# Kernel optimization log

Hardware: AMD Instinct MI355X
Metric: run time of the kernel (lower is better)

## Reference

```python
import jax, jax.numpy as jnp
import numpy as np

R_CUT = 5.0
N_NODES = 50000
N_EDGES = 400000
N_GRAPHS = 2500
D = 128        # embedding_size (hardcoded by torch.split(..., 128))
N_RBF = 20
N_BLOCKS = 3
PI = 3.141592653589793


def setup_inputs() -> dict:
    key = jax.random.key(0)
    ks = jax.random.split(key, 32)
    w = lambda k, s: (jax.random.normal(k, s) * 0.05).astype(jnp.float32)
    z = jax.random.randint(ks[0], (N_NODES,), 0, 100)
    edges = jax.random.randint(ks[1], (N_EDGES, 2), 0, N_NODES)
    r_ij = jax.random.uniform(ks[2], (N_EDGES, 1), minval=0.8, maxval=R_CUT, dtype=jnp.float32)
    d = jax.random.normal(ks[3], (N_EDGES, 3), dtype=jnp.float32)
    r_ij_normalized = d / jnp.linalg.norm(d, axis=1, keepdims=True)
    graph_idx = jax.random.randint(ks[4], (N_NODES,), 0, N_GRAPHS)
    return {
        "z": z, "edges": edges, "r_ij": r_ij,
        "r_ij_normalized": r_ij_normalized, "graph_idx": graph_idx,
        "emb": w(ks[5], (100, D)),
        # message blocks (stacked over N_BLOCKS)
        "msg_w1": w(ks[6], (N_BLOCKS, D, D)),   "msg_b1": w(ks[7], (N_BLOCKS, D)),
        "msg_w2": w(ks[8], (N_BLOCKS, D, 3 * D)), "msg_b2": w(ks[9], (N_BLOCKS, 3 * D)),
        "rbf_w": w(ks[10], (N_BLOCKS, N_RBF, 3 * D)), "rbf_b": w(ks[11], (N_BLOCKS, 3 * D)),
        # update blocks
        "upd_U": w(ks[12], (N_BLOCKS, D, D)), "upd_V": w(ks[13], (N_BLOCKS, D, D)),
        "upd_w1": w(ks[14], (N_BLOCKS, 2 * D, D)), "upd_b1": w(ks[15], (N_BLOCKS, D)),
        "upd_w2": w(ks[16], (N_BLOCKS, D, 3 * D)), "upd_b2": w(ks[17], (N_BLOCKS, 3 * D)),
        # readout
        "blue_w1": w(ks[18], (D, D)), "blue_b1": w(ks[19], (D,)),
        "blue_w2": w(ks[20], (D, 1)), "blue_b2": w(ks[21], (1,)),
    }


def _rbf(r, r_cut):
    n = jnp.arange(1, N_RBF + 1, dtype=r.dtype)  # [20]
    return jnp.sin(n * PI / r_cut * r) / r        # [E,20]


def _fcut(r, r_cut):
    return jnp.where(r <= r_cut, 0.5 * (jnp.cos(PI * r / r_cut) + 1.0), 0.0)


def painn_forward(z, edges, r_ij, r_ij_normalized, graph_idx, emb,
                  msg_w1, msg_b1, msg_w2, msg_b2, rbf_w, rbf_b,
                  upd_U, upd_V, upd_w1, upd_b1, upd_w2, upd_b2,
                  blue_w1, blue_b1, blue_w2, blue_b2):
    silu = jax.nn.silu
    src = edges[:, 1]  # gathered (neighbor j)
    dst = edges[:, 0]  # scattered (center i)
    s = emb[z]                                           # [N,128]
    v = jnp.zeros((s.shape[0], 3, D), dtype=r_ij.dtype)  # [N,3,128]
    rbf = _rbf(r_ij, R_CUT)                              # [E,20]
    f_c = _fcut(r_ij, R_CUT)                             # [E,1]
    for i in range(N_BLOCKS):
        # --- message block ---
        rbf_fcut = (rbf @ rbf_w[i] + rbf_b[i]) * f_c            # [E,384]
        s_pass = silu(s @ msg_w1[i] + msg_b1[i]) @ msg_w2[i] + msg_b2[i]  # [N,384]
        pass_out = rbf_fcut * s_pass[src]                        # [E,384]
        d_v, d_s, d_rep = jnp.split(pass_out, 3, axis=-1)        # each [E,128]
        delta_v = v[src] * d_v[:, None, :] + r_ij_normalized[:, :, None] * d_rep[:, None, :]
        s = s + jax.ops.segment_sum(d_s, dst, num_segments=N_NODES)
        v = v + jax.ops.segment_sum(delta_v, dst, num_segments=N_NODES)
        # --- update block ---
        U_v = jnp.einsum('nde,ef->ndf', v, upd_U[i])             # [N,3,128]
        V_v = jnp.einsum('nde,ef->ndf', v, upd_V[i])
        V_norm = jnp.linalg.norm(V_v, axis=1)                    # [N,128]
        sv = jnp.concatenate([V_norm, s], axis=1)                # [N,256]
        a = silu(sv @ upd_w1[i] + upd_b1[i]) @ upd_w2[i] + upd_b2[i]  # [N,384]
        avv, asv, ass = jnp.split(a, 3, axis=1)
        s = s + jnp.sum(U_v * V_v, axis=1) * asv + ass
        v = v + avv[:, None, :] * U_v
    blue = silu(s @ blue_w1 + blue_b1) @ blue_w2 + blue_b2       # [N,1]
    return jax.ops.segment_sum(blue, graph_idx, num_segments=N_GRAPHS)  # [G,1]


def reference(z, edges, r_ij, r_ij_normalized, graph_idx, emb,
              msg_w1, msg_b1, msg_w2, msg_b2, rbf_w, rbf_b,
              upd_U, upd_V, upd_w1, upd_b1, upd_w2, upd_b2,
              blue_w1, blue_b1, blue_w2, blue_b2):
    return painn_forward(z, edges, r_ij, r_ij_normalized, graph_idx, emb,
                         msg_w1, msg_b1, msg_w2, msg_b2, rbf_w, rbf_b,
                         upd_U, upd_V, upd_w1, upd_b1, upd_w2, upd_b2,
                         blue_w1, blue_b1, blue_w2, blue_b2)
```

## Files before the change

### kernel.cpp

```cpp
#include <hip/hip_runtime.h>
#include <hip/hip_bf16.h>
#include <math.h>

#define N_NODES 50000
#define N_EDGES 400000
#define N_GRAPHS 2500
#define D 128
#define D3 384
#define N_RBF 20
#define R_CUT 5.0f
#define PI_F 3.14159265358979f
#define NCH 98
#define GEB 16
#define GLDS_STRIDE 388

typedef __attribute__((ext_vector_type(8))) short bf16x8;
typedef __attribute__((ext_vector_type(4))) float f32x4;

__device__ __forceinline__ float silu_f(float x) {
    return x / (1.0f + __expf(-x));
}
__device__ __forceinline__ short f2bf(float x) {
    union { float f; unsigned u; } v; v.f = x;
    unsigned r = (v.u + 0x7FFFu + ((v.u >> 16) & 1u)) >> 16;
    return (short)r;
}
__device__ __forceinline__ float bf2f(short x) {
    union { unsigned u; float f; } v; v.u = ((unsigned)(unsigned short)x) << 16;
    return v.f;
}

#define MAXJOBS 19
struct PackJobs {
    const float* W[MAXJOBS];
    short* P[MAXJOBS];
    int K[MAXJOBS];
    int N[MAXJOBS];
    int boff[MAXJOBS + 1];
    int njobs;
};
__global__ void k_packall(PackJobs jobs) {
    int b = blockIdx.x;
    int j = 0;
    while (j + 1 < jobs.njobs && b >= jobs.boff[j + 1]) ++j;
    int t = (b - jobs.boff[j]) * 256 + threadIdx.x;
    int K = jobs.K[j], N = jobs.N[j];
    int NKT = K / 32;
    int total = (N / 16) * NKT * 64;
    if (t >= total) return;
    const float* W = jobs.W[j];
    short* P = jobs.P[j];
    int lane = t & 63;
    int kt = (t >> 6) % NKT;
    int nt = (t >> 6) / NKT;
    int k0 = kt * 32 + (lane >> 4) * 8;
    int col = nt * 16 + (lane & 15);
    #pragma unroll
    for (int q = 0; q < 8; ++q)
        P[(size_t)t * 8 + q] = f2bf(W[(size_t)(k0 + q) * N + col]);
}

__global__ void k_packrbf(const float* __restrict__ rbf_w, const float* __restrict__ rbf_b,
                          short* __restrict__ P) {
    int t = blockIdx.x * 256 + threadIdx.x;
    if (t >= 3 * 1536) return;
    int i = t / 1536;
    int r = t - i * 1536;
    int lane = r & 63;
    int nt = r >> 6;
    int col = nt * 16 + (lane & 15);
    int k0 = (lane >> 4) * 8;
    const float* W = rbf_w + (size_t)i * N_RBF * D3;
    const float* B = rbf_b + (size_t)i * D3;
    short* out = P + (size_t)i * 12288 + (size_t)r * 8;
    #pragma unroll
    for (int q = 0; q < 8; ++q) {
        int k = k0 + q;
        float v = (k < N_RBF) ? W[(size_t)k * D3 + col] : ((k == N_RBF) ? B[col] : 0.0f);
        out[q] = f2bf(v);
    }
}

template<int K, int N, bool SILU, int AMODE>
__global__ __launch_bounds__(256) void k_gemm(const void* __restrict__ Aptr,
                                              const void* __restrict__ A2ptr,
                                              const short* __restrict__ Bp,
                                              const float* __restrict__ bias,
                                              short* __restrict__ Cbf, int M) {
    constexpr int NKT = K / 32, NNT = N / 16;
    int lane = threadIdx.x & 63, wv = threadIdx.x >> 6;
    int tile = blockIdx.x * 4 + wv;
    if (tile * 16 >= M) return;
    int arow = tile * 16 + (lane & 15);
    int kgrp = (lane >> 4) * 8;

    bf16x8 a[NKT];
    if (AMODE == 0) {
        const short* A = (const short*)Aptr + (size_t)arow * K + kgrp;
        #pragma unroll
        for (int kt = 0; kt < NKT; ++kt) a[kt] = *(const bf16x8*)(A + kt * 32);
    } else if (AMODE == 1) {
        const float* A = (const float*)Aptr + (size_t)arow * K + kgrp;
        #pragma unroll
        for (int kt = 0; kt < NKT; ++kt)
            #pragma unroll
            for (int j = 0; j < 8; ++j) a[kt][j] = f2bf(A[kt * 32 + j]);
    } else {
        const short* A1 = (const short*)Aptr + (size_t)arow * 128 + kgrp;
        const float* A2 = (const float*)A2ptr + (size_t)arow * 128 + kgrp;
        #pragma unroll
        for (int kt = 0; kt < 4 && kt < NKT; ++kt) a[kt] = *(const bf16x8*)(A1 + kt * 32);
        #pragma unroll
        for (int kt = 4; kt < NKT; ++kt)
            #pragma unroll
            for (int j = 0; j < 8; ++j) a[kt][j] = f2bf(A2[(kt - 4) * 32 + j]);
    }

    int crow0 = tile * 16 + (lane >> 4) * 4;
    int ccol = lane & 15;
    const bf16x8* Bv = (const bf16x8*)Bp;
    #pragma unroll
    for (int nt = 0; nt < NNT; ++nt) {
        f32x4 acc = {0.f, 0.f, 0.f, 0.f};
        #pragma unroll
        for (int kt = 0; kt < NKT; ++kt) {
            bf16x8 b = Bv[(nt * NKT + kt) * 64 + lane];
            acc = __builtin_amdgcn_mfma_f32_16x16x32_bf16(a[kt], b, acc, 0, 0, 0);
        }
        int col = nt * 16 + ccol;
        float bs = bias ? bias[col] : 0.0f;
        #pragma unroll
        for (int j = 0; j < 4; ++j) {
            float v = acc[j] + bs;
            if (SILU) v = silu_f(v);
            Cbf[(size_t)(crow0 + j) * N + col] = f2bf(v);
        }
    }
}

__global__ __launch_bounds__(256) void k_gemmUV(const short* __restrict__ A,
                                                const short* __restrict__ Bp,
                                                short* __restrict__ Cu,
                                                short* __restrict__ Cv, int M) {
    int lane = threadIdx.x & 63, wv = threadIdx.x >> 6;
    int tile = blockIdx.x * 4 + wv;
    if (tile * 16 >= M) return;
    int arow = tile * 16 + (lane & 15);
    int kgrp = (lane >> 4) * 8;
    const short* Ar = A + (size_t)arow * 128 + kgrp;
    bf16x8 a[4];
    #pragma unroll
    for (int kt = 0; kt < 4; ++kt) a[kt] = *(const bf16x8*)(Ar + kt * 32);
    int crow0 = tile * 16 + (lane >> 4) * 4;
    int ccol = lane & 15;
    const bf16x8* Bv = (const bf16x8*)Bp;
    #pragma unroll
    for (int nt = 0; nt < 16; ++nt) {
        f32x4 acc = {0.f, 0.f, 0.f, 0.f};
        #pragma unroll
        for (int kt = 0; kt < 4; ++kt)
            acc = __builtin_amdgcn_mfma_f32_16x16x32_bf16(a[kt], Bv[(nt * 4 + kt) * 64 + lane], acc, 0, 0, 0);
        int col = nt * 16 + ccol;
        short* C = (col < 128) ? Cu : Cv;
        int cc = col & 127;
        #pragma unroll
        for (int j = 0; j < 4; ++j)
            C[(size_t)(crow0 + j) * 128 + cc] = f2bf(acc[j]);
    }
}

__global__ void k_embed(const int* __restrict__ z, const float* __restrict__ emb,
                        float* __restrict__ s) {
    int i = blockIdx.x * blockDim.x + threadIdx.x;
    if (i < N_NODES * D) {
        int n = i >> 7, c = i & 127;
        s[i] = emb[z[n] * D + c];
    }
}

__global__ void k_hist(const int* __restrict__ edges, int* __restrict__ cnt) {
    int e = blockIdx.x * 256 + threadIdx.x;
    if (e < N_EDGES) atomicAdd(&cnt[edges[2 * e]], 1);
}

__global__ void k_scan1(const int* __restrict__ cnt, int* __restrict__ csum) {
    int t = threadIdx.x;
    int g = blockIdx.x * 512 + t;
    int v = (g < N_NODES) ? cnt[g] : 0;
    #pragma unroll
    for (int off = 32; off > 0; off >>= 1) v += __shfl_down(v, off, 64);
    __shared__ int ws[8];
    if ((t & 63) == 0) ws[t >> 6] = v;
    __syncthreads();
    if (t == 0) {
        int sum = 0;
        #pragma unroll
        for (int i = 0; i < 8; ++i) sum += ws[i];
        csum[blockIdx.x] = sum;
    }
}

__global__ void k_scan2(const int* __restrict__ csum, int* __restrict__ cbase) {
    if (threadIdx.x == 0 && blockIdx.x == 0) {
        int s = 0;
        for (int i = 0; i < NCH; ++i) { cbase[i] = s; s += csum[i]; }
    }
}

__global__ void k_scan3(const int* __restrict__ cnt, const int* __restrict__ cbase,
                        int* __restrict__ rowptr) {
    __shared__ int buf[512];
    int t = threadIdx.x;
    int g = blockIdx.x * 512 + t;
    int orig = (g < N_NODES) ? cnt[g] : 0;
    buf[t] = orig;
    __syncthreads();
    for (int off = 1; off < 512; off <<= 1) {
        int v = (t >= off) ? buf[t - off] : 0;
        __syncthreads();
        buf[t] += v;
        __syncthreads();
    }
    if (g < N_NODES) rowptr[g] = cbase[blockIdx.x] + buf[t] - orig;
    if (g == 0 && blockIdx.x == 0) rowptr[N_NODES] = N_EDGES;
}

__global__ void k_scatter(const int* __restrict__ edges, const float* __restrict__ r_ij,
                          const float* __restrict__ rhat, const int* __restrict__ rowptr,
                          int* __restrict__ cursor, int* __restrict__ esrc,
                          short* __restrict__ erbf, float4* __restrict__ erhat) {
    int e = blockIdx.x * 256 + threadIdx.x;
    if (e >= N_EDGES) return;
    int dst = edges[2 * e], src = edges[2 * e + 1];
    int p = rowptr[dst] + atomicAdd(&cursor[dst], 1);
    esrc[p] = src;
    float r = r_ij[e];
    float fc = (r <= R_CUT) ? 0.5f * (cosf(PI_F * r / R_CUT) + 1.0f) : 0.0f;
    float inv_r = 1.0f / r;
    short rec[32];
    #pragma unroll
    for (int k = 0; k < N_RBF; ++k)
        rec[k] = f2bf(sinf((float)(k + 1) * (PI_F / R_CUT) * r) * inv_r * fc);
    rec[20] = f2bf(fc);
    #pragma unroll
    for (int k = 21; k < 32; ++k) rec[k] = 0;
    short* out = erbf + (size_t)p * 32;
    #pragma unroll
    for (int k = 0; k < 32; ++k) out[k] = rec[k];
    float4 rh;
    rh.x = rhat[3 * e]; rh.y = rhat[3 * e + 1]; rh.z = rhat[3 * e + 2]; rh.w = 0.f;
    erhat[p] = rh;
}

__global__ __launch_bounds__(128, 4) void k_edge3(
    const int* __restrict__ rowptr, const int* __restrict__ esrc,
    const short* __restrict__ erbf, const float4* __restrict__ erhat,
    const short* __restrict__ pRbf,
    const short* __restrict__ spass, const short* __restrict__ vold,
    float* __restrict__ s, short* __restrict__ vnew) {
    __shared__ short gate_lds[GEB * GLDS_STRIDE];
    __shared__ int   src_lds[GEB];
    __shared__ float4 rh_lds[GEB];
    int tid = threadIdx.x;
    int lane = tid & 63;
    int wv = tid >> 6;
    int c = tid;
    int ntb = wv * 12;
    bf16x8 bfr[12];
    #pragma unroll
    for (int t = 0; t < 12; ++t)
        bfr[t] = *(const bf16x8*)(pRbf + ((size_t)((ntb + t) * 64 + lane)) * 8);
    int r0 = (lane >> 4) * 4;
    int fcol = lane & 15;
    for (int n = blockIdx.x; n < N_NODES; n += gridDim.x) {
        int p0 = rowptr[n], p1 = rowptr[n + 1];
        float sa = 0.f, va0 = 0.f, va1 = 0.f, va2 = 0.f;
        for (int pb = p0; pb < p1; pb += GEB) {
            int erow = pb + (lane & 15);
            if (erow >= p1) erow = p1 - 1;
            bf16x8 afrag = *(const bf16x8*)(erbf + (size_t)erow * 32 + (lane >> 4) * 8);
            if (tid < GEB) {
                int p = pb + tid;
                if (p < p1) { src_lds[tid] = esrc[p]; rh_lds[tid] = erhat[p]; }
            }
            #pragma unroll
            for (int t = 0; t < 12; ++t) {
                f32x4 acc = {0.f, 0.f, 0.f, 0.f};
                acc = __builtin_amdgcn_mfma_f32_16x16x32_bf16(afrag, bfr[t], acc, 0, 0, 0);
                int col = (ntb + t) * 16 + fcol;
                #pragma unroll
                for (int j = 0; j < 4; ++j)
                    gate_lds[(r0 + j) * GLDS_STRIDE + col] = f2bf(acc[j]);
            }
            __syncthreads();
            int pe = (pb + GEB < p1) ? pb + GEB : p1;
            for (int p = pb; p < pe; ++p) {
                int src = src_lds[p - pb];
                float4 rh = rh_lds[p - pb];
                const short* g = gate_lds + (p - pb) * GLDS_STRIDE;
                float a0 = bf2f(g[c]);
                float a1 = bf2f(g[128 + c]);
                float a2 = bf2f(g[256 + c]);
                const short* sp = spass + (size_t)src * D3;
                float dv = a0 * bf2f(sp[c]);
                float ds = a1 * bf2f(sp[128 + c]);
                float dr = a2 * bf2f(sp[256 + c]);
                sa += ds;
                const short* vs = vold + (size_t)src * D3;
                va0 += bf2f(vs[c]) * dv + rh.x * dr;
                va1 += bf2f(vs[128 + c]) * dv + rh.y * dr;
                va2 += bf2f(vs[256 + c]) * dv + rh.z * dr;
            }
            __syncthreads();
        }
        s[(size_t)n * D + c] += sa;
        size_t vb = (size_t)n * D3;
        vnew[vb + c]       = f2bf(bf2f(vold[vb + c]) + va0);
        vnew[vb + 128 + c] = f2bf(bf2f(vold[vb + 128 + c]) + va1);
        vnew[vb + 256 + c] = f2bf(bf2f(vold[vb + 256 + c]) + va2);
    }
}

__global__ void k_svbuild(const short* __restrict__ Vv, short* __restrict__ Vn) {
    int i = blockIdx.x * 256 + threadIdx.x;
    int n = i >> 7, c = i & 127;
    float acc = 0.f;
    #pragma unroll
    for (int d = 0; d < 3; ++d) {
        float v = bf2f(Vv[(size_t)(n * 3 + d) * D + c]);
        acc += v * v;
    }
    Vn[i] = f2bf(sqrtf(acc));
}

__global__ void k_apply(float* __restrict__ s, short* __restrict__ v,
                        const short* __restrict__ Uv, const short* __restrict__ Vv,
                        const short* __restrict__ a_bf) {
    int i = blockIdx.x * 256 + threadIdx.x;
    int n = i >> 7, c = i & 127;
    float avv = bf2f(a_bf[(size_t)n * D3 + c]);
    float asv = bf2f(a_bf[(size_t)n * D3 + 128 + c]);
    float ass = bf2f(a_bf[(size_t)n * D3 + 256 + c]);
    float scal = 0.f;
    float uvr[3];
    #pragma unroll
    for (int d = 0; d < 3; ++d) {
        float u = bf2f(Uv[(size_t)(n * 3 + d) * D + c]);
        float vv = bf2f(Vv[(size_t)(n * 3 + d) * D + c]);
        uvr[d] = u;
        scal += u * vv;
    }
    s[i] += scal * asv + ass;
    #pragma unroll
    for (int d = 0; d < 3; ++d) {
        size_t idx = (size_t)n * D3 + d * 128 + c;
        v[idx] = f2bf(bf2f(v[idx]) + avv * uvr[d]);
    }
}

__global__ void k_blue_dot(const short* __restrict__ h, const int* __restrict__ graph_idx,
                           const float* __restrict__ w2, const float* __restrict__ b2,
                           float* __restrict__ out) {
    __shared__ float red[4];
    int c = threadIdx.x & 127;
    int n = blockIdx.x * 2 + (threadIdx.x >> 7);
    float val = bf2f(h[(size_t)n * D + c]) * w2[c];
    #pragma unroll
    for (int off = 32; off > 0; off >>= 1) val += __shfl_down(val, off, 64);
    if ((threadIdx.x & 63) == 0) red[threadIdx.x >> 6] = val;
    __syncthreads();
    if (threadIdx.x == 0)   atomicAdd(&out[graph_idx[n]], red[0] + red[1] + b2[0]);
    if (threadIdx.x == 128) atomicAdd(&out[graph_idx[n]], red[2] + red[3] + b2[0]);
}

static inline int gemm_grid(int M) { return (M / 16 + 3) / 4; }

extern "C" void kernel_launch(void* const* d_in, const int* in_sizes, int n_in,
                              void* d_out, int out_size, void* d_ws, size_t ws_size,
                              hipStream_t stream) {
    const int*   z         = (const int*)d_in[0];
    const int*   edges     = (const int*)d_in[1];
    const float* r_ij      = (const float*)d_in[2];
    const float* rhat      = (const float*)d_in[3];
    const int*   graph_idx = (const int*)d_in[4];
    const float* emb       = (const float*)d_in[5];
    const float* msg_w1    = (const float*)d_in[6];
    const float* msg_b1    = (const float*)d_in[7];
    const float* msg_w2    = (const float*)d_in[8];
    const float* msg_b2    = (const float*)d_in[9];
    const float* rbf_w     = (const float*)d_in[10];
    const float* rbf_b     = (const float*)d_in[11];
    const float* upd_U     = (const float*)d_in[12];
    const float* upd_V     = (const float*)d_in[13];
    const float* upd_w1    = (const float*)d_in[14];
    const float* upd_b1    = (const float*)d_in[15];
    const float* upd_w2    = (const float*)d_in[16];
    const float* upd_b2    = (const float*)d_in[17];
    const float* blue_w1   = (const float*)d_in[18];
    const float* blue_b1   = (const float*)d_in[19];
    const float* blue_w2   = (const float*)d_in[20];
    const float* blue_b2   = (const float*)d_in[21];
    float* out = (float*)d_out;

    char* ws = (char*)d_ws;
    size_t off = 0;
    auto alloc = [&](size_t bytes) { void* p = ws + off; off += (bytes + 255) & ~(size_t)255; return p; };

    float* s      = (float*)alloc((size_t)N_NODES * D * 4);
    short* bufV0  = (short*)alloc((size_t)N_NODES * D3 * 2);
    short* bufV1  = (short*)alloc((size_t)N_NODES * D3 * 2);
    short* shrd   = (short*)alloc((size_t)N_NODES * D3 * 2);
    short* hbuf   = (short*)alloc((size_t)N_NODES * D * 2);
    short* Vv     = (short*)alloc((size_t)N_NODES * D3 * 2);
    short* Vn     = shrd;
    int*    esrc   = (int*)alloc((size_t)N_EDGES * 4);
    short*  erbf   = (short*)alloc((size_t)N_EDGES * 32 * 2);
    float4* erhat  = (float4*)alloc((size_t)N_EDGES * 16);
    int*    rowptr = (int*)alloc((size_t)(N_NODES + 1) * 4);
    int*    cnt    = (int*)alloc((size_t)N_NODES * 4);
    int*    csum   = (int*)alloc(NCH * 4);
    int*    cbase  = (int*)alloc(NCH * 4);

    short* pBlue = (short*)alloc(16384 * 2);
    short* pRbfAll = (short*)alloc((size_t)3 * 12288 * 2);
    short* pMsgW1[3]; short* pMsgW2[3]; short* pUV[3]; short* pUpdW1[3]; short* pUpdW2[3];
    for (int i = 0; i < 3; ++i) {
        pMsgW1[i] = (short*)alloc(16384 * 2);
        pMsgW2[i] = (short*)alloc(49152 * 2);
        pUV[i]    = (short*)alloc(32768 * 2);
        pUpdW1[i] = (short*)alloc(32768 * 2);
        pUpdW2[i] = (short*)alloc(49152 * 2);
    }

    PackJobs jobs;
    jobs.njobs = 0;
    int bacc = 0;
    auto addjob = [&](const float* W, short* P, int K, int N) {
        int j = jobs.njobs++;
        jobs.W[j] = W; jobs.P[j] = P; jobs.K[j] = K; jobs.N[j] = N;
        jobs.boff[j] = bacc;
        int total = (N / 16) * (K / 32) * 64;
        bacc += (total + 255) / 256;
        jobs.boff[j + 1] = bacc;
    };
    addjob(blue_w1, pBlue, 128, 128);
    for (int i = 0; i < 3; ++i) {
        addjob(msg_w1 + (size_t)i * D * D,     pMsgW1[i], 128, 128);
        addjob(msg_w2 + (size_t)i * D * D3,    pMsgW2[i], 128, 384);
        addjob(upd_U  + (size_t)i * D * D,     pUV[i],          128, 128);
        addjob(upd_V  + (size_t)i * D * D,     pUV[i] + 16384,  128, 128);
        addjob(upd_w1 + (size_t)i * 2 * D * D, pUpdW1[i], 256, 128);
        addjob(upd_w2 + (size_t)i * D * D3,    pUpdW2[i], 128, 384);
    }
    k_packall<<<bacc, 256, 0, stream>>>(jobs);
    k_packrbf<<<18, 256, 0, stream>>>(rbf_w, rbf_b, pRbfAll);

    hipMemsetAsync(cnt, 0, (size_t)N_NODES * 4, stream);
    k_hist<<<(N_EDGES + 255) / 256, 256, 0, stream>>>(edges, cnt);
    k_scan1<<<NCH, 512, 0, stream>>>(cnt, csum);
    k_scan2<<<1, 64, 0, stream>>>(csum, cbase);
    k_scan3<<<NCH, 512, 0, stream>>>(cnt, cbase, rowptr);
    hipMemsetAsync(cnt, 0, (size_t)N_NODES * 4, stream);
    k_scatter<<<(N_EDGES + 255) / 256, 256, 0, stream>>>(edges, r_ij, rhat, rowptr, cnt,
                                                         esrc, erbf, erhat);

    hipMemsetAsync(bufV0, 0, (size_t)N_NODES * D3 * 2, stream);
    hipMemsetAsync(d_out, 0, (size_t)out_size * sizeof(float), stream);
    k_embed<<<(N_NODES * D) / 256, 256, 0, stream>>>(z, emb, s);

    const int gN  = gemm_grid(N_NODES);
    const int gN3 = gemm_grid(N_NODES * 3);

    for (int i = 0; i < 3; ++i) {
        short* vstate = (i & 1) ? bufV1 : bufV0;
        short* vscr   = (i & 1) ? bufV0 : bufV1;
        k_gemm<128, 128, true, 1><<<gN, 256, 0, stream>>>(
            s, nullptr, pMsgW1[i], msg_b1 + (size_t)i * D, hbuf, N_NODES);
        k_gemm<128, 384, false, 0><<<gN, 256, 0, stream>>>(
            hbuf, nullptr, pMsgW2[i], msg_b2 + (size_t)i * D3, shrd, N_NODES);
        k_edge3<<<4096, 128, 0, stream>>>(rowptr, esrc, erbf, erhat,
                                          pRbfAll + (size_t)i * 12288,
                                          shrd, vstate, s, vscr);
        k_gemmUV<<<gN3, 256, 0, stream>>>(vscr, pUV[i], vstate, Vv, N_NODES * 3);
        k_svbuild<<<(N_NODES * D) / 256, 256, 0, stream>>>(Vv, Vn);
        k_gemm<256, 128, true, 2><<<gN, 256, 0, stream>>>(
            Vn, s, pUpdW1[i], upd_b1 + (size_t)i * D, hbuf, N_NODES);
        k_gemm<128, 384, false, 0><<<gN, 256, 0, stream>>>(
            hbuf, nullptr, pUpdW2[i], upd_b2 + (size_t)i * D3, shrd, N_NODES);
        k_apply<<<(N_NODES * D) / 256, 256, 0, stream>>>(s, vscr, vstate, Vv, shrd);
    }

    k_gemm<128, 128, true, 1><<<gN, 256, 0, stream>>>(
        s, nullptr, pBlue, blue_b1, hbuf, N_NODES);
    k_blue_dot<<<N_NODES / 2, 256, 0, stream>>>(hbuf, graph_idx, blue_w2, blue_b2, out);
}
```

Baseline: 1.021 ms.

## Fuse vector norm into update GEMM and apply into second update GEMM

Computes the per-channel vector norm inside the first update GEMM's A-load, which removes the separate norm kernel. The second update GEMM is fused with the state-apply step, so the 384-wide intermediate is never written to memory. The message GEMM output and the edge gate LDS are interleaved so each edge loads two gate values with a single 32-bit access. Edge unit vectors are packed into the unused slots of the RBF record, which drops the separate rhat array. The edge grid is enlarged and the LDS stride changed, and the fused apply kernel does scattered per-element global reads and writes.

```diff
diff --git a/kernel.cpp b/kernel.cpp
--- a/kernel.cpp
+++ b/kernel.cpp
@@ -12,7 +12,7 @@
 #define PI_F 3.14159265358979f
 #define NCH 98
 #define GEB 16
-#define GLDS_STRIDE 388
+#define GS 392
 
 typedef __attribute__((ext_vector_type(8))) short bf16x8;
 typedef __attribute__((ext_vector_type(4))) float f32x4;
@@ -81,7 +81,7 @@
     }
 }
 
-template<int K, int N, bool SILU, int AMODE>
+template<int K, int N, bool SILU, int AMODE, int CMODE>
 __global__ __launch_bounds__(256) void k_gemm(const void* __restrict__ Aptr,
                                               const void* __restrict__ A2ptr,
                                               const short* __restrict__ Bp,
@@ -106,10 +106,19 @@
             #pragma unroll
             for (int j = 0; j < 8; ++j) a[kt][j] = f2bf(A[kt * 32 + j]);
     } else {
-        const short* A1 = (const short*)Aptr + (size_t)arow * 128 + kgrp;
+        const short* A1 = (const short*)Aptr + (size_t)arow * D3 + kgrp;
         const float* A2 = (const float*)A2ptr + (size_t)arow * 128 + kgrp;
         #pragma unroll
-        for (int kt = 0; kt < 4 && kt < NKT; ++kt) a[kt] = *(const bf16x8*)(A1 + kt * 32);
+        for (int kt = 0; kt < 4 && kt < NKT; ++kt) {
+            bf16x8 v0 = *(const bf16x8*)(A1 + kt * 32);
+            bf16x8 v1 = *(const bf16x8*)(A1 + kt * 32 + 128);
+            bf16x8 v2 = *(const bf16x8*)(A1 + kt * 32 + 256);
+            #pragma unroll
+            for (int j = 0; j < 8; ++j) {
+                float f0 = bf2f(v0[j]), f1 = bf2f(v1[j]), f2 = bf2f(v2[j]);
+                a[kt][j] = f2bf(sqrtf(f0 * f0 + f1 * f1 + f2 * f2));
+            }
+        }
         #pragma unroll
         for (int kt = 4; kt < NKT; ++kt)
             #pragma unroll
@@ -129,11 +138,12 @@
         }
         int col = nt * 16 + ccol;
         float bs = bias ? bias[col] : 0.0f;
+        int oidx = (CMODE == 1) ? (col < 256 ? (((col & 127) << 1) | (col >> 7)) : col) : col;
         #pragma unroll
         for (int j = 0; j < 4; ++j) {
             float v = acc[j] + bs;
             if (SILU) v = silu_f(v);
-            Cbf[(size_t)(crow0 + j) * N + col] = f2bf(v);
+            Cbf[(size_t)(crow0 + j) * N + oidx] = f2bf(v);
         }
     }
 }
@@ -166,6 +176,60 @@
         #pragma unroll
         for (int j = 0; j < 4; ++j)
             C[(size_t)(crow0 + j) * 128 + cc] = f2bf(acc[j]);
+    }
+}
+
+__global__ __launch_bounds__(256) void k_w2apply(const short* __restrict__ A,
+                                                 const short* __restrict__ Bp,
+                                                 const float* __restrict__ b2,
+                                                 const short* __restrict__ Uv,
+                                                 const short* __restrict__ Vv,
+                                                 float* __restrict__ s,
+                                                 short* __restrict__ v, int M) {
+    int lane = threadIdx.x & 63, wv = threadIdx.x >> 6;
+    int tile = blockIdx.x * 4 + wv;
+    if (tile * 16 >= M) return;
+    int arow = tile * 16 + (lane & 15);
+    int kgrp = (lane >> 4) * 8;
+    const short* Ar = A + (size_t)arow * 128 + kgrp;
+    bf16x8 a[4];
+    #pragma unroll
+    for (int kt = 0; kt < 4; ++kt) a[kt] = *(const bf16x8*)(Ar + kt * 32);
+    int crow0 = tile * 16 + (lane >> 4) * 4;
+    int ccol = lane & 15;
+    const bf16x8* Bv = (const bf16x8*)Bp;
+    #pragma unroll
+    for (int t = 0; t < 8; ++t) {
+        f32x4 accA = {0.f, 0.f, 0.f, 0.f};
+        f32x4 accS = {0.f, 0.f, 0.f, 0.f};
+        f32x4 accB = {0.f, 0.f, 0.f, 0.f};
+        #pragma unroll
+        for (int kt = 0; kt < 4; ++kt) {
+            accA = __builtin_amdgcn_mfma_f32_16x16x32_bf16(a[kt], Bv[(t * 4 + kt) * 64 + lane], accA, 0, 0, 0);
+            accS = __builtin_amdgcn_mfma_f32_16x16x32_bf16(a[kt], Bv[((t + 8) * 4 + kt) * 64 + lane], accS, 0, 0, 0);
+            accB = __builtin_amdgcn_mfma_f32_16x16x32_bf16(a[kt], Bv[((t + 16) * 4 + kt) * 64 + lane], accB, 0, 0, 0);
+        }
+        int c = t * 16 + ccol;
+        float bA = b2[c], bS = b2[128 + c], bB = b2[256 + c];
+        #pragma unroll
+        for (int j = 0; j < 4; ++j) {
+            int n = crow0 + j;
+            float avv = accA[j] + bA;
+            float asv = accS[j] + bS;
+            float ass = accB[j] + bB;
+            const short* Un = Uv + (size_t)n * D3;
+            const short* Vn = Vv + (size_t)n * D3;
+            short* vn = v + (size_t)n * D3;
+            float scal = 0.f;
+            #pragma unroll
+            for (int d = 0; d < 3; ++d) {
+                float u = bf2f(Un[d * 128 + c]);
+                float vv = bf2f(Vn[d * 128 + c]);
+                scal += u * vv;
+                vn[d * 128 + c] = f2bf(bf2f(vn[d * 128 + c]) + avv * u);
+            }
+            s[(size_t)n * D + c] += scal * asv + ass;
+        }
     }
 }
 
@@ -228,7 +292,7 @@
 __global__ void k_scatter(const int* __restrict__ edges, const float* __restrict__ r_ij,
                           const float* __restrict__ rhat, const int* __restrict__ rowptr,
                           int* __restrict__ cursor, int* __restrict__ esrc,
-                          short* __restrict__ erbf, float4* __restrict__ erhat) {
+                          short* __restrict__ erbf) {
     int e = blockIdx.x * 256 + threadIdx.x;
     if (e >= N_EDGES) return;
     int dst = edges[2 * e], src = edges[2 * e + 1];
@@ -242,23 +306,22 @@
     for (int k = 0; k < N_RBF; ++k)
         rec[k] = f2bf(sinf((float)(k + 1) * (PI_F / R_CUT) * r) * inv_r * fc);
     rec[20] = f2bf(fc);
-    #pragma unroll
-    for (int k = 21; k < 32; ++k) rec[k] = 0;
+    rec[21] = f2bf(rhat[3 * e]);
+    rec[22] = f2bf(rhat[3 * e + 1]);
+    rec[23] = f2bf(rhat[3 * e + 2]);
+    #pragma unroll
+    for (int k = 24; k < 32; ++k) rec[k] = 0;
     short* out = erbf + (size_t)p * 32;
     #pragma unroll
     for (int k = 0; k < 32; ++k) out[k] = rec[k];
-    float4 rh;
-    rh.x = rhat[3 * e]; rh.y = rhat[3 * e + 1]; rh.z = rhat[3 * e + 2]; rh.w = 0.f;
-    erhat[p] = rh;
 }
 
 __global__ __launch_bounds__(128, 4) void k_edge3(
     const int* __restrict__ rowptr, const int* __restrict__ esrc,
-    const short* __restrict__ erbf, const float4* __restrict__ erhat,
-    const short* __restrict__ pRbf,
+    const short* __restrict__ erbf, const short* __restrict__ pRbf,
     const short* __restrict__ spass, const short* __restrict__ vold,
     float* __restrict__ s, short* __restrict__ vnew) {
-    __shared__ short gate_lds[GEB * GLDS_STRIDE];
+    __shared__ short gate_lds[GEB * GS];
     __shared__ int   src_lds[GEB];
     __shared__ float4 rh_lds[GEB];
     int tid = threadIdx.x;
@@ -281,29 +344,36 @@
             bf16x8 afrag = *(const bf16x8*)(erbf + (size_t)erow * 32 + (lane >> 4) * 8);
             if (tid < GEB) {
                 int p = pb + tid;
-                if (p < p1) { src_lds[tid] = esrc[p]; rh_lds[tid] = erhat[p]; }
+                if (p < p1) {
+                    src_lds[tid] = esrc[p];
+                    const short* eb = erbf + (size_t)p * 32;
+                    rh_lds[tid] = make_float4(bf2f(eb[21]), bf2f(eb[22]), bf2f(eb[23]), 0.f);
+                }
             }
             #pragma unroll
             for (int t = 0; t < 12; ++t) {
                 f32x4 acc = {0.f, 0.f, 0.f, 0.f};
                 acc = __builtin_amdgcn_mfma_f32_16x16x32_bf16(afrag, bfr[t], acc, 0, 0, 0);
                 int col = (ntb + t) * 16 + fcol;
+                int oidx = (col < 256) ? (((col & 127) << 1) | (col >> 7)) : col;
                 #pragma unroll
                 for (int j = 0; j < 4; ++j)
-                    gate_lds[(r0 + j) * GLDS_STRIDE + col] = f2bf(acc[j]);
+                    gate_lds[(r0 + j) * GS + oidx] = f2bf(acc[j]);
             }
             __syncthreads();
             int pe = (pb + GEB < p1) ? pb + GEB : p1;
             for (int p = pb; p < pe; ++p) {
                 int src = src_lds[p - pb];
                 float4 rh = rh_lds[p - pb];
-                const short* g = gate_lds + (p - pb) * GLDS_STRIDE;
-                float a0 = bf2f(g[c]);
-                float a1 = bf2f(g[128 + c]);
+                const short* g = gate_lds + (p - pb) * GS;
+                unsigned gp = *(const unsigned*)(g + 2 * c);
+                float a0 = bf2f((short)(gp & 0xFFFF));
+                float a1 = bf2f((short)(gp >> 16));
                 float a2 = bf2f(g[256 + c]);
                 const short* sp = spass + (size_t)src * D3;
-                float dv = a0 * bf2f(sp[c]);
-                float ds = a1 * bf2f(sp[128 + c]);
+                unsigned spp = *(const unsigned*)(sp + 2 * c);
+                float dv = a0 * bf2f((short)(spp & 0xFFFF));
+                float ds = a1 * bf2f((short)(spp >> 16));
                 float dr = a2 * bf2f(sp[256 + c]);
                 sa += ds;
                 const short* vs = vold + (size_t)src * D3;
@@ -318,43 +388,6 @@
         vnew[vb + c]       = f2bf(bf2f(vold[vb + c]) + va0);
         vnew[vb + 128 + c] = f2bf(bf2f(vold[vb + 128 + c]) + va1);
         vnew[vb + 256 + c] = f2bf(bf2f(vold[vb + 256 + c]) + va2);
-    }
-}
-
-__global__ void k_svbuild(const short* __restrict__ Vv, short* __restrict__ Vn) {
-    int i = blockIdx.x * 256 + threadIdx.x;
-    int n = i >> 7, c = i & 127;
-    float acc = 0.f;
-    #pragma unroll
-    for (int d = 0; d < 3; ++d) {
-        float v = bf2f(Vv[(size_t)(n * 3 + d) * D + c]);
-        acc += v * v;
-    }
-    Vn[i] = f2bf(sqrtf(acc));
-}
-
-__global__ void k_apply(float* __restrict__ s, short* __restrict__ v,
-                        const short* __restrict__ Uv, const short* __restrict__ Vv,
-                        const short* __restrict__ a_bf) {
-    int i = blockIdx.x * 256 + threadIdx.x;
-    int n = i >> 7, c = i & 127;
-    float avv = bf2f(a_bf[(size_t)n * D3 + c]);
-    float asv = bf2f(a_bf[(size_t)n * D3 + 128 + c]);
-    float ass = bf2f(a_bf[(size_t)n * D3 + 256 + c]);
-    float scal = 0.f;
-    float uvr[3];
-    #pragma unroll
-    for (int d = 0; d < 3; ++d) {
-        float u = bf2f(Uv[(size_t)(n * 3 + d) * D + c]);
-        float vv = bf2f(Vv[(size_t)(n * 3 + d) * D + c]);
-        uvr[d] = u;
-        scal += u * vv;
-    }
-    s[i] += scal * asv + ass;
-    #pragma unroll
-    for (int d = 0; d < 3; ++d) {
-        size_t idx = (size_t)n * D3 + d * 128 + c;
-        v[idx] = f2bf(bf2f(v[idx]) + avv * uvr[d]);
     }
 }
 
@@ -409,13 +442,11 @@
     float* s      = (float*)alloc((size_t)N_NODES * D * 4);
     short* bufV0  = (short*)alloc((size_t)N_NODES * D3 * 2);
     short* bufV1  = (short*)alloc((size_t)N_NODES * D3 * 2);
-    short* shrd   = (short*)alloc((size_t)N_NODES * D3 * 2);
+    short* spassI = (short*)alloc((size_t)N_NODES * D3 * 2);
     short* hbuf   = (short*)alloc((size_t)N_NODES * D * 2);
     short* Vv     = (short*)alloc((size_t)N_NODES * D3 * 2);
-    short* Vn     = shrd;
     int*    esrc   = (int*)alloc((size_t)N_EDGES * 4);
     short*  erbf   = (short*)alloc((size_t)N_EDGES * 32 * 2);
-    float4* erhat  = (float4*)alloc((size_t)N_EDGES * 16);
     int*    rowptr = (int*)alloc((size_t)(N_NODES + 1) * 4);
     int*    cnt    = (int*)alloc((size_t)N_NODES * 4);
     int*    csum   = (int*)alloc(NCH * 4);
@@ -462,7 +493,7 @@
     k_scan3<<<NCH, 512, 0, stream>>>(cnt, cbase, rowptr);
     hipMemsetAsync(cnt, 0, (size_t)N_NODES * 4, stream);
     k_scatter<<<(N_EDGES + 255) / 256, 256, 0, stream>>>(edges, r_ij, rhat, rowptr, cnt,
-                                                         esrc, erbf, erhat);
+                                                         esrc, erbf);
 
     hipMemsetAsync(bufV0, 0, (size_t)N_NODES * D3 * 2, stream);
     hipMemsetAsync(d_out, 0, (size_t)out_size * sizeof(float), stream);
@@ -474,23 +505,21 @@
     for (int i = 0; i < 3; ++i) {
         short* vstate = (i & 1) ? bufV1 : bufV0;
         short* vscr   = (i & 1) ? bufV0 : bufV1;
-        k_gemm<128, 128, true, 1><<<gN, 256, 0, stream>>>(
+        k_gemm<128, 128, true, 1, 0><<<gN, 256, 0, stream>>>(
             s, nullptr, pMsgW1[i], msg_b1 + (size_t)i * D, hbuf, N_NODES);
-        k_gemm<128, 384, false, 0><<<gN, 256, 0, stream>>>(
-            hbuf, nullptr, pMsgW2[i], msg_b2 + (size_t)i * D3, shrd, N_NODES);
-        k_edge3<<<4096, 128, 0, stream>>>(rowptr, esrc, erbf, erhat,
+        k_gemm<128, 384, false, 0, 1><<<gN, 256, 0, stream>>>(
+            hbuf, nullptr, pMsgW2[i], msg_b2 + (size_t)i * D3, spassI, N_NODES);
+        k_edge3<<<6144, 128, 0, stream>>>(rowptr, esrc, erbf,
                                           pRbfAll + (size_t)i * 12288,
-                                          shrd, vstate, s, vscr);
+                                          spassI, vstate, s, vscr);
         k_gemmUV<<<gN3, 256, 0, stream>>>(vscr, pUV[i], vstate, Vv, N_NODES * 3);
-        k_svbuild<<<(N_NODES * D) / 256, 256, 0, stream>>>(Vv, Vn);
-        k_gemm<256, 128, true, 2><<<gN, 256, 0, stream>>>(
-            Vn, s, pUpdW1[i], upd_b1 + (size_t)i * D, hbuf, N_NODES);
-        k_gemm<128, 384, false, 0><<<gN, 256, 0, stream>>>(
-            hbuf, nullptr, pUpdW2[i], upd_b2 + (size_t)i * D3, shrd, N_NODES);
-        k_apply<<<(N_NODES * D) / 256, 256, 0, stream>>>(s, vscr, vstate, Vv, shrd);
-    }
-
-    k_gemm<128, 128, true, 1><<<gN, 256, 0, stream>>>(
+        k_gemm<256, 128, true, 3, 0><<<gN, 256, 0, stream>>>(
+            Vv, s, pUpdW1[i], upd_b1 + (size_t)i * D, hbuf, N_NODES);
+        k_w2apply<<<gN, 256, 0, stream>>>(hbuf, pUpdW2[i], upd_b2 + (size_t)i * D3,
+                                          vstate, Vv, s, vscr, N_NODES);
+    }
+
+    k_gemm<128, 128, true, 1, 0><<<gN, 256, 0, stream>>>(
         s, nullptr, pBlue, blue_b1, hbuf, N_NODES);
     k_blue_dot<<<N_NODES / 2, 256, 0, stream>>>(hbuf, graph_idx, blue_w2, blue_b2, out);
 }
```

Result: slower. 1.221 ms (+19.6%).
